# Optimization experiments

Hardware: AMD Instinct MI355X
Metric: run time of the kernel (lower is better)

## Reference

```python
import jax, jax.numpy as jnp
import numpy as np

B, J, C = 4096, 17, 512       # batch, joints (length), channels (dim)
K, TOK, CH, H, KS, G = 3, 64, 1024, 8, 3, 8  # adj kernels, tokens_dim, channels_dim, heads, conv_large, gn groups
EPS = 1e-5


def setup_inputs() -> dict:
    key = jax.random.key(0)
    ks = jax.random.split(key, 16)
    r = lambda i, shp, s=0.02: jax.random.normal(ks[i], shp, jnp.float32) * s
    return {
        "x": jax.random.normal(ks[0], (B, J, C), jnp.float32),
        "adj": jax.random.uniform(ks[1], (K, J, J), jnp.float32) / J,
        "norm1_w": jnp.ones((J,), jnp.float32), "norm1_b": jnp.zeros((J,), jnp.float32),
        "gcn1_w": r(2, (K * C, C)), "gcn1_b": jnp.zeros((K * C,), jnp.float32),
        "dw_w": r(3, (C, 1, KS), 0.1), "dw_b": jnp.zeros((C,), jnp.float32),
        "gn1_w": jnp.ones((C,), jnp.float32), "gn1_b": jnp.zeros((C,), jnp.float32),
        "pw_w": r(4, (C, C)), "pw_b": jnp.zeros((C,), jnp.float32),
        "mlp1_w1": r(5, (TOK, J)), "mlp1_b1": jnp.zeros((TOK,), jnp.float32),
        "mlp1_w2": r(6, (J, TOK)), "mlp1_b2": jnp.zeros((J,), jnp.float32),
        "qkv_w": r(7, (3 * C, C)), "qkv_b": jnp.zeros((3 * C,), jnp.float32),
        "proj_w": r(8, (C, C)), "proj_b": jnp.zeros((C,), jnp.float32),
        "gnf_w": jnp.ones((C,), jnp.float32), "gnf_b": jnp.zeros((C,), jnp.float32),
        "norm2_w": jnp.ones((C,), jnp.float32), "norm2_b": jnp.zeros((C,), jnp.float32),
        "mlp2_w1": r(9, (CH, C)), "mlp2_b1": jnp.zeros((CH,), jnp.float32),
        "mlp2_w2": r(10, (C, CH)), "mlp2_b2": jnp.zeros((C,), jnp.float32),
        "gcn2_w": r(11, (K * C, C)), "gcn2_b": jnp.zeros((K * C,), jnp.float32),
    }


def _gelu(t):
    return jax.nn.gelu(t, approximate=False)  # torch nn.GELU default is exact erf


def _ln(t, w, b):  # LayerNorm over last axis
    m = t.mean(-1, keepdims=True)
    v = ((t - m) ** 2).mean(-1, keepdims=True)
    return (t - m) * jax.lax.rsqrt(v + EPS) * w + b


def _gn(t, w, b):  # GroupNorm(G, C) over (B, C, J)
    Bn, Cc, Jn = t.shape
    r = t.reshape(Bn, G, -1)
    m = r.mean(-1, keepdims=True)
    v = ((r - m) ** 2).mean(-1, keepdims=True)
    r = (r - m) * jax.lax.rsqrt(v + EPS)
    return r.reshape(Bn, Cc, Jn) * w[:, None] + b[:, None]


def _gcn(t, w, b, adj):  # t: (B,C,J); 1x1 conv to K*C then einsum with adj (K,J,J)
    y = jnp.einsum('bcj,oc->boj', t, w) + b[:, None]
    y = y.reshape(t.shape[0], K, C, t.shape[2])
    return jnp.einsum('bkcv,kvw->bcw', y, adj)


def reference(x, adj, norm1_w, norm1_b, gcn1_w, gcn1_b, dw_w, dw_b, gn1_w, gn1_b,
              pw_w, pw_b, mlp1_w1, mlp1_b1, mlp1_w2, mlp1_b2, qkv_w, qkv_b,
              proj_w, proj_b, gnf_w, gnf_b, norm2_w, norm2_b,
              mlp2_w1, mlp2_b1, mlp2_w2, mlp2_b2, gcn2_w, gcn2_b):
    res = x                                   # (B,J,C)
    xc = jnp.swapaxes(x, 1, 2)                # (B,C,J)
    xc = _ln(xc, norm1_w, norm1_b)            # LayerNorm over joints

    # --- branch 1: GCN ---
    x_gcn1 = _gcn(xc, gcn1_w, gcn1_b, adj)    # (B,C,J)

    # --- branch 2: depthwise conv + token MLP ---
    h = jax.lax.conv_general_dilated(xc, dw_w, (1,), [(KS // 2, KS // 2)],
                                     dimension_numbers=('NCH', 'OIH', 'NCH'),
                                     feature_group_count=C) + dw_b[:, None]
    h = _gelu(_gn(h, gn1_w, gn1_b))
    h = jnp.einsum('bcj,oc->boj', h, pw_w) + pw_b[:, None]      # 1x1 conv
    h = _gelu(jnp.einsum('bcj,tj->bct', h, mlp1_w1) + mlp1_b1)  # token mlp fc1
    h = jnp.einsum('bct,jt->bcj', h, mlp1_w2) + mlp1_b2         # token mlp fc2

    # --- branch 3: global spatial attention over joints ---
    dh = C // H
    qkv = jnp.einsum('bcj,oc->boj', xc, qkv_w) + qkv_b[:, None]  # (B,3C,J)
    q, k_, v_ = jnp.split(qkv, 3, axis=1)
    q = q.reshape(-1, H, dh, J); k_ = k_.reshape(-1, H, dh, J); v_ = v_.reshape(-1, H, dh, J)
    attn = jax.nn.softmax(jnp.einsum('bhdi,bhdj->bhij', q, k_) / jnp.sqrt(jnp.float32(dh)), axis=-1)
    sga = jnp.einsum('bhij,bhdj->bhdi', attn, v_).reshape(-1, C, J)
    sga = jnp.einsum('bcj,oc->boj', sga, proj_w) + proj_b[:, None]

    # --- fuse ---
    xc = _gelu(_gn(sga + x_gcn1 + h, gnf_w, gnf_b))
    xj = jnp.swapaxes(xc, 1, 2)               # (B,J,C)
    res_channel = xj
    xn = _ln(xj + res, norm2_w, norm2_b)      # LayerNorm over channels
    m = _gelu(jnp.einsum('bjc,hc->bjh', xn, mlp2_w1) + mlp2_b1)
    m = jnp.einsum('bjh,ch->bjc', m, mlp2_w2) + mlp2_b2
    g2 = _gcn(jnp.swapaxes(m, 1, 2), gcn2_w, gcn2_b, adj)  # (B,C,J)
    xj = res_channel + jnp.swapaxes(g2, 1, 2)
    return xj + res
```

## Files before the change

### kernel.cpp

```cpp
#include <hip/hip_runtime.h>
#include <stdint.h>

#define BB 4096
#define JJ 17
#define CC 512

typedef unsigned short u16;
typedef __bf16 bf16x8 __attribute__((ext_vector_type(8)));
typedef float  f32x4  __attribute__((ext_vector_type(4)));
typedef float  f32x2  __attribute__((ext_vector_type(2)));

__device__ __forceinline__ float bf2f(u16 u){ return __uint_as_float(((uint32_t)u)<<16); }
__device__ __forceinline__ u16 f2bf(float f){
  uint32_t u = __float_as_uint(f);
  u += 0x7fffu + ((u>>16)&1u);
  return (u16)(u>>16);
}
__device__ __forceinline__ void unpk2(uint32_t u, float& lo, float& hi){
  lo = __uint_as_float(u<<16);
  hi = __uint_as_float(u & 0xffff0000u);
}
__device__ __forceinline__ float gelu_f(float x){
  float x2 = x*x;
  float y2 = x*fmaf(0.0713548162726f, x2, 1.59576912161f);
  float ey = __builtin_amdgcn_exp2f(y2*1.44269504089f);
  return fmaf(-x, __builtin_amdgcn_rcpf(ey+1.f), x);
}
__device__ __forceinline__ void pkfma(f32x2& d, f32x2 a, f32x2 b){
  asm volatile("v_pk_fma_f32 %0, %1, %2, %0" : "+v"(d) : "v"(a), "v"(b));
}
__device__ __forceinline__ void gll16(const void* g, void* l){
  __builtin_amdgcn_global_load_lds(
      (const __attribute__((address_space(1))) void*)g,
      (__attribute__((address_space(3))) void*)l, 16, 0, 0);
}

__global__ void k_cvt(const float* __restrict__ in, u16* __restrict__ out, int n){
  int i = blockIdx.x*blockDim.x + threadIdx.x;
  if (i < n) out[i] = f2bf(in[i]);
}

__global__ void k_tokprep(const float* __restrict__ w1, const float* __restrict__ w2,
                          float* __restrict__ w1p, float* __restrict__ w2p){
  int i = blockIdx.x*blockDim.x + threadIdx.x;
  if (i >= 1280) return;
  int t = i/20, j = i%20;
  w1p[i] = (j<17) ? w1[t*17+j] : 0.f;
  w2p[i] = (j<17) ? w2[j*64+t] : 0.f;
}

__global__ __launch_bounds__(512) void k_pre(
    const float* __restrict__ x, int b0,
    const float* __restrict__ n1w, const float* __restrict__ n1b,
    const float* __restrict__ dww, const float* __restrict__ dwb,
    const float* __restrict__ gn1w, const float* __restrict__ gn1b,
    u16* __restrict__ xc, u16* __restrict__ hgn)
{
  int b = blockIdx.x, c = threadIdx.x;
  const float* xp = x + (size_t)(b0+b)*JJ*CC + c;
  float v[JJ]; float s = 0.f;
  #pragma unroll
  for (int j=0;j<JJ;j++){ v[j] = xp[(size_t)j*CC]; s += v[j]; }
  float mn = s*(1.f/JJ); float var = 0.f;
  #pragma unroll
  for (int j=0;j<JJ;j++){ float d=v[j]-mn; var += d*d; }
  float rr = rsqrtf(var*(1.f/JJ)+1e-5f);
  float xcv[JJ];
  #pragma unroll
  for (int j=0;j<JJ;j++) xcv[j] = (v[j]-mn)*rr*n1w[j] + n1b[j];
  u16* xo = xc + (size_t)b*JJ*CC + c;
  #pragma unroll
  for (int j=0;j<JJ;j++) xo[(size_t)j*CC] = f2bf(xcv[j]);
  float w0=dww[c*3+0], w1=dww[c*3+1], w2=dww[c*3+2], db=dwb[c];
  float h[JJ];
  #pragma unroll
  for (int j=0;j<JJ;j++){
    float a = db + w1*xcv[j];
    if (j>0)    a += w0*xcv[j-1];
    if (j<JJ-1) a += w2*xcv[j+1];
    h[j] = a;
  }
  float ss=0.f, sq=0.f;
  #pragma unroll
  for (int j=0;j<JJ;j++){ ss += h[j]; sq += h[j]*h[j]; }
  for (int off=32; off; off>>=1){ ss += __shfl_xor(ss,off); sq += __shfl_xor(sq,off); }
  float gm = ss*(1.f/(64.f*JJ));
  float gr = rsqrtf(sq*(1.f/(64.f*JJ)) - gm*gm + 1e-5f);
  float gw = gn1w[c], gb = gn1b[c];
  u16* ho = hgn + (size_t)b*JJ*CC + c;
  #pragma unroll
  for (int j=0;j<JJ;j++){
    float t = (h[j]-gm)*gr*gw + gb;
    ho[(size_t)j*CC] = f2bf(gelu_f(t));
  }
}

template<int DO_GELU, int DO_ADD>
__global__ __launch_bounds__(512,2) void gemm256(
    const u16* __restrict__ A, const u16* __restrict__ W, const float* __restrict__ bias,
    u16* __restrict__ out, const u16* __restrict__ add0, const u16* __restrict__ add1,
    int M, int N, int K, int NXT)
{
  __shared__ __align__(16) u16 lds[65536];
  const int tid  = threadIdx.x;
  const int wid  = tid>>6, lane = tid&63;

  const int nwg = gridDim.x;
  const int q8 = nwg>>3, r8 = nwg&7;
  const int xcd = blockIdx.x & 7, sub = blockIdx.x >> 3;
  const int wg = (xcd<r8 ? xcd*(q8+1) : r8*(q8+1)+(xcd-r8)*q8) + sub;
  const int n0 = (wg % NXT)*256;
  const int m0 = (wg / NXT)*256;

  const int wm = wid>>2, wn = wid&3;
  const int lr = lane&15, lg = lane>>4;
  const int T  = K>>6;
  const int K64 = K<<6;

  const int rg = tid>>3, g = tid&7;
  const int gswS = (g ^ (rg&7))<<3;
  const u16* gA = A + (size_t)(m0+rg)*K + gswS;
  const u16* gB = W + (size_t)(n0+rg)*K + gswS;
  const int stl = wid*512;

  const int gsw0 = ((0+lg) ^ (lr&7))<<3;
  const int gsw1 = ((4+lg) ^ (lr&7))<<3;
  const int rowA0 = wm*128 + lr;
  const int rowB0 = wn*64  + lr;

  f32x4 acc[8][4];
  #pragma unroll
  for (int i=0;i<8;i++)
    #pragma unroll
    for (int j=0;j<4;j++) acc[i][j] = (f32x4){0.f,0.f,0.f,0.f};

  bf16x8 av[2][4], bv0[2][2], bv1[2][2];

  auto STAGE = [&](const u16* ga, const u16* gb, int bufo){
    u16* la = lds + bufo + stl;
    u16* lb = lds + 32768 + bufo + stl;
    gll16(ga,        la);
    gll16(ga+K64,    la+4096);
    gll16(ga+2*K64,  la+8192);
    gll16(ga+3*K64,  la+12288);
    gll16(gb,        lb);
    gll16(gb+K64,    lb+4096);
    gll16(gb+2*K64,  lb+8192);
    gll16(gb+3*K64,  lb+12288);
  };
  auto LDA = [&](int qm, int bufo){
    #pragma unroll
    for (int i=0;i<4;i++){
      const int rb = bufo + (rowA0 + qm*64 + i*16)*64;
      av[0][i] = *(const bf16x8*)&lds[rb + gsw0];
      av[1][i] = *(const bf16x8*)&lds[rb + gsw1];
    }
  };
  auto LDB = [&](int qn, int bufo, bf16x8 (&bv)[2][2]){
    #pragma unroll
    for (int j=0;j<2;j++){
      const int rb = 32768 + bufo + (rowB0 + qn*32 + j*16)*64;
      bv[0][j] = *(const bf16x8*)&lds[rb + gsw0];
      bv[1][j] = *(const bf16x8*)&lds[rb + gsw1];
    }
  };
  auto MF = [&](int qm, int qn, bf16x8 (&bv)[2][2]){
    __builtin_amdgcn_s_setprio(1);
    #pragma unroll
    for (int kk=0;kk<2;kk++)
      #pragma unroll
      for (int i=0;i<4;i++)
        #pragma unroll
        for (int j=0;j<2;j++)
          acc[qm*4+i][qn*2+j] = __builtin_amdgcn_mfma_f32_16x16x32_bf16(
              av[kk][i], bv[kk][j], acc[qm*4+i][qn*2+j], 0,0,0);
    __builtin_amdgcn_s_setprio(0);
  };

  STAGE(gA, gB, 0);
  asm volatile("s_waitcnt vmcnt(0)" ::: "memory");
  __builtin_amdgcn_s_barrier();
  __builtin_amdgcn_sched_barrier(0);

  const u16* gAn = gA + 64;
  const u16* gBn = gB + 64;
  for (int t=0; t<T; ++t){
    const int bufo = (t&1)<<14;
    if (t+1 < T){
      STAGE(gAn, gBn, ((t+1)&1)<<14);
      gAn += 64; gBn += 64;
    }
    LDA(0, bufo); LDB(0, bufo, bv0);
    asm volatile("s_waitcnt lgkmcnt(0)" ::: "memory");
    __builtin_amdgcn_sched_barrier(0);
    MF(0,0,bv0);
    __builtin_amdgcn_s_barrier();
    LDB(1, bufo, bv1);
    asm volatile("s_waitcnt lgkmcnt(0)" ::: "memory");
    __builtin_amdgcn_sched_barrier(0);
    MF(0,1,bv1);
    __builtin_amdgcn_s_barrier();
    LDA(1, bufo);
    asm volatile("s_waitcnt lgkmcnt(0)" ::: "memory");
    __builtin_amdgcn_sched_barrier(0);
    MF(1,0,bv0);
    __builtin_amdgcn_s_barrier();
    MF(1,1,bv1);
    asm volatile("s_waitcnt vmcnt(0)" ::: "memory");
    __builtin_amdgcn_s_barrier();
    __builtin_amdgcn_sched_barrier(0);
  }

  const int rbase = lg*4;
  #pragma unroll
  for (int mi=0; mi<8; mi++){
    #pragma unroll
    for (int ni=0; ni<4; ni++){
      const int col  = n0 + wn*64 + ni*16 + lr;
      const int row0 = m0 + wm*128 + mi*16 + rbase;
      const float bvl = bias[col];
      #pragma unroll
      for (int r=0;r<4;r++){
        size_t idx = (size_t)(row0+r)*N + col;
        float v = acc[mi][ni][r] + bvl;
        if (DO_ADD)  v += bf2f(add0[idx]) + bf2f(add1[idx]);
        if (DO_GELU) v = gelu_f(v);
        out[idx] = f2bf(v);
      }
    }
  }
}

template<int FINAL>
__global__ __launch_bounds__(512) void k_gcn2(
    const u16* __restrict__ G, const float* __restrict__ adj,
    u16* __restrict__ xg,
    const u16* __restrict__ rc, const float* __restrict__ x, int b0,
    float* __restrict__ out)
{
  __shared__ __align__(16) float adjp[51*20];
  const int tid = threadIdx.x;
  for (int i=tid; i<1020; i+=512){
    int r=i/20, cl=i%20;
    adjp[i] = (cl<17) ? adj[r*17+cl] : 0.f;
  }
  __syncthreads();

  const int sl  = tid>>7;
  const int l   = tid&127;
  const int c0  = l*4;
  const int bl  = blockIdx.x*4 + sl;

  float acc[JJ][4];
  #pragma unroll
  for (int w=0;w<JJ;w++)
    #pragma unroll
    for (int e=0;e<4;e++) acc[w][e]=0.f;

  const u16* gbase = G + (size_t)bl*JJ*1536 + c0;
  #pragma unroll 3
  for (int kv=0; kv<51; kv++){
    const int k = kv/JJ, v = kv - k*JJ;
    uint2 yu = *(const uint2*)(gbase + (size_t)v*1536 + k*512);
    float y0,y1,y2,y3;
    unpk2(yu.x, y0, y1);
    unpk2(yu.y, y2, y3);
    const f32x4* arow = (const f32x4*)&adjp[kv*20];
    f32x4 a0=arow[0], a1=arow[1], a2=arow[2], a3=arow[3];
    float a16 = adjp[kv*20+16];
    float ar[JJ] = {a0[0],a0[1],a0[2],a0[3], a1[0],a1[1],a1[2],a1[3],
                    a2[0],a2[1],a2[2],a2[3], a3[0],a3[1],a3[2],a3[3], a16};
    #pragma unroll
    for (int w=0;w<JJ;w++){
      acc[w][0] += y0*ar[w];
      acc[w][1] += y1*ar[w];
      acc[w][2] += y2*ar[w];
      acc[w][3] += y3*ar[w];
    }
  }

  if (FINAL==0){
    u16* xo = xg + (size_t)bl*JJ*CC + c0;
    #pragma unroll
    for (int w=0;w<JJ;w++){
      uint2 o;
      o.x = (uint32_t)f2bf(acc[w][0]) | ((uint32_t)f2bf(acc[w][1])<<16);
      o.y = (uint32_t)f2bf(acc[w][2]) | ((uint32_t)f2bf(acc[w][3])<<16);
      *(uint2*)(xo + (size_t)w*CC) = o;
    }
  } else {
    const size_t gb = (size_t)(b0+bl)*JJ*CC + c0;
    const u16* rp = rc + (size_t)bl*JJ*CC + c0;
    #pragma unroll
    for (int w=0;w<JJ;w++){
      uint2 ru = *(const uint2*)(rp + (size_t)w*CC);
      float r0,r1,r2,r3;
      unpk2(ru.x, r0, r1);
      unpk2(ru.y, r2, r3);
      f32x4 xv = *(const f32x4*)(x + gb + (size_t)w*CC);
      f32x4 o;
      o[0]=acc[w][0]+r0+xv[0]; o[1]=acc[w][1]+r1+xv[1];
      o[2]=acc[w][2]+r2+xv[2]; o[3]=acc[w][3]+r3+xv[3];
      *(f32x4*)(out + gb + (size_t)w*CC) = o;
    }
  }
}

__global__ __launch_bounds__(512) void k_attn(const u16* __restrict__ Gqkv, u16* __restrict__ sga){
  __shared__ __align__(16) u16 qs[8*17*72];
  __shared__ __align__(16) u16 ks_[8*17*72];
  __shared__ __align__(16) float at[8*17*20];
  int b = blockIdx.x, tid = threadIdx.x;
  int h = tid>>6, d = tid&63;
  const u16* base = Gqkv + (size_t)b*JJ*1536;
  float vv[JJ];
  #pragma unroll
  for (int i=0;i<JJ;i++){
    qs [(h*JJ+i)*72 + d] = base[(size_t)i*1536 +        h*64 + d];
    ks_[(h*JJ+i)*72 + d] = base[(size_t)i*1536 +  512 + h*64 + d];
    vv[i] = bf2f(base[(size_t)i*1536 + 1024 + h*64 + d]);
  }
  __syncthreads();
  for (int p=d; p<289; p+=64){
    int i=p/JJ, j=p-i*JJ;
    const u16* qrow = &qs [(h*JJ+i)*72];
    const u16* krow = &ks_[(h*JJ+j)*72];
    float a=0.f;
    #pragma unroll
    for (int t=0;t<8;t++){
      bf16x8 q8 = *(const bf16x8*)&qrow[t*8];
      bf16x8 k8 = *(const bf16x8*)&krow[t*8];
      #pragma unroll
      for (int e=0;e<8;e++) a += (float)q8[e]*(float)k8[e];
    }
    at[(h*JJ+i)*20 + j] = a*0.125f;
  }
  __syncthreads();
  if (d < JJ){
    float* row = &at[(h*JJ+d)*20];
    f32x4 r0=((f32x4*)row)[0], r1=((f32x4*)row)[1], r2=((f32x4*)row)[2], r3=((f32x4*)row)[3];
    float e16=row[16];
    float rv[JJ]={r0[0],r0[1],r0[2],r0[3],r1[0],r1[1],r1[2],r1[3],
                  r2[0],r2[1],r2[2],r2[3],r3[0],r3[1],r3[2],r3[3],e16};
    float mx=-1e30f;
    #pragma unroll
    for (int j=0;j<JJ;j++) mx=fmaxf(mx,rv[j]);
    float sm=0.f;
    #pragma unroll
    for (int j=0;j<JJ;j++){ rv[j]=__builtin_amdgcn_exp2f((rv[j]-mx)*1.44269504089f); sm+=rv[j]; }
    float inv=1.f/sm;
    #pragma unroll
    for (int j=0;j<JJ;j++) row[j]=rv[j]*inv;
  }
  __syncthreads();
  #pragma unroll
  for (int i=0;i<JJ;i++){
    const float* row = &at[(h*JJ+i)*20];
    f32x4 r0=((const f32x4*)row)[0], r1=((const f32x4*)row)[1],
          r2=((const f32x4*)row)[2], r3=((const f32x4*)row)[3];
    float a = r0[0]*vv[0]+r0[1]*vv[1]+r0[2]*vv[2]+r0[3]*vv[3]
            + r1[0]*vv[4]+r1[1]*vv[5]+r1[2]*vv[6]+r1[3]*vv[7]
            + r2[0]*vv[8]+r2[1]*vv[9]+r2[2]*vv[10]+r2[3]*vv[11]
            + r3[0]*vv[12]+r3[1]*vv[13]+r3[2]*vv[14]+r3[3]*vv[15]
            + row[16]*vv[16];
    sga[((size_t)b*JJ+i)*CC + h*64 + d] = f2bf(a);
  }
}

__global__ __launch_bounds__(512) void k_tok(const u16* __restrict__ Hpw,
    const float* __restrict__ w1p, const float* __restrict__ w2p,
    const float* __restrict__ b1, const float* __restrict__ b2,
    u16* __restrict__ h2o){
  __shared__ __align__(16) float w1s[1280], w2s[1280];
  __shared__ float b1s[64], b2s[20];
  const int tid = threadIdx.x;
  for (int i=tid; i<1280; i+=512){ w1s[i]=w1p[i]; w2s[i]=w2p[i]; }
  if (tid<64) b1s[tid]=b1[tid];
  if (tid<20) b2s[tid] = (tid<17) ? b2[tid] : 0.f;
  __syncthreads();

  const int bl = blockIdx.x*2 + (tid>>8);
  const int c0 = tid&255;
  const u16* hp = Hpw + (size_t)bl*JJ*CC;
  float hv0[JJ], hv1[JJ];
  #pragma unroll
  for (int j=0;j<JJ;j++){
    hv0[j]=bf2f(hp[(size_t)j*CC + c0]);
    hv1[j]=bf2f(hp[(size_t)j*CC + c0 + 256]);
  }
  f32x2 h0p[9], h1p[9];
  #pragma unroll
  for (int p=0;p<8;p++){
    h0p[p] = (f32x2){hv0[2*p], hv0[2*p+1]};
    h1p[p] = (f32x2){hv1[2*p], hv1[2*p+1]};
  }
  h0p[8] = (f32x2){hv0[16], 0.f};
  h1p[8] = (f32x2){hv1[16], 0.f};

  f32x2 a20[9], a21[9];
  #pragma unroll
  for (int p=0;p<9;p++){
    f32x2 bb = (f32x2){b2s[2*p], b2s[2*p+1]};
    a20[p]=bb; a21[p]=bb;
  }

  for (int t=0;t<64;t++){
    f32x4 wa = *(const f32x4*)&w1s[t*20];
    f32x4 wb = *(const f32x4*)&w1s[t*20+4];
    f32x4 wc = *(const f32x4*)&w1s[t*20+8];
    f32x4 wd = *(const f32x4*)&w1s[t*20+12];
    float  we = w1s[t*20+16];
    f32x2 wp[9] = {(f32x2){wa[0],wa[1]},(f32x2){wa[2],wa[3]},
                   (f32x2){wb[0],wb[1]},(f32x2){wb[2],wb[3]},
                   (f32x2){wc[0],wc[1]},(f32x2){wc[2],wc[3]},
                   (f32x2){wd[0],wd[1]},(f32x2){wd[2],wd[3]},
                   (f32x2){we,0.f}};
    f32x2 s0 = (f32x2){b1s[t], 0.f};
    f32x2 s1 = s0;
    #pragma unroll
    for (int p=0;p<9;p++){ pkfma(s0, h0p[p], wp[p]); pkfma(s1, h1p[p], wp[p]); }
    float a0 = gelu_f(s0[0] + s0[1]);
    float a1 = gelu_f(s1[0] + s1[1]);
    wa = *(const f32x4*)&w2s[t*20];
    wb = *(const f32x4*)&w2s[t*20+4];
    wc = *(const f32x4*)&w2s[t*20+8];
    wd = *(const f32x4*)&w2s[t*20+12];
    we = w2s[t*20+16];
    f32x2 wq[9] = {(f32x2){wa[0],wa[1]},(f32x2){wa[2],wa[3]},
                   (f32x2){wb[0],wb[1]},(f32x2){wb[2],wb[3]},
                   (f32x2){wc[0],wc[1]},(f32x2){wc[2],wc[3]},
                   (f32x2){wd[0],wd[1]},(f32x2){wd[2],wd[3]},
                   (f32x2){we,0.f}};
    f32x2 a0b = (f32x2){a0,a0};
    f32x2 a1b = (f32x2){a1,a1};
    #pragma unroll
    for (int p=0;p<9;p++){ pkfma(a20[p], a0b, wq[p]); pkfma(a21[p], a1b, wq[p]); }
  }
  u16* ho = h2o + (size_t)bl*JJ*CC;
  #pragma unroll
  for (int j=0;j<JJ;j++){
    ho[(size_t)j*CC + c0]       = f2bf(a20[j>>1][j&1]);
    ho[(size_t)j*CC + c0 + 256] = f2bf(a21[j>>1][j&1]);
  }
}

__global__ __launch_bounds__(512) void k_fuse(const u16* __restrict__ s,
    const float* __restrict__ x, int b0,
    const float* __restrict__ gfw, const float* __restrict__ gfb,
    const float* __restrict__ n2w, const float* __restrict__ n2b,
    u16* __restrict__ rc, u16* __restrict__ xn){
  __shared__ float rS[8][JJ], rQ[8][JJ];
  int b = blockIdx.x, c = threadIdx.x;
  int wave = c>>6, lane = c&63;
  const u16* sp = s + (size_t)b*JJ*CC + c;
  float sv[JJ];
  #pragma unroll
  for (int j=0;j<JJ;j++) sv[j]=bf2f(sp[(size_t)j*CC]);
  float ss=0.f, sq=0.f;
  #pragma unroll
  for (int j=0;j<JJ;j++){ ss+=sv[j]; sq+=sv[j]*sv[j]; }
  for (int off=32; off; off>>=1){ ss += __shfl_xor(ss,off); sq += __shfl_xor(sq,off); }
  float gm = ss*(1.f/1088.f);
  float gr = rsqrtf(sq*(1.f/1088.f) - gm*gm + 1e-5f);
  float gw=gfw[c], gb=gfb[c];
  const float* xp = x + (size_t)(b0+b)*JJ*CC + c;
  u16* rp = rc + (size_t)b*JJ*CC + c;
  float t[JJ];
  #pragma unroll
  for (int j=0;j<JJ;j++){
    float v = gelu_f((sv[j]-gm)*gr*gw + gb);
    rp[(size_t)j*CC] = f2bf(v);
    t[j] = v + xp[(size_t)j*CC];
  }
  #pragma unroll
  for (int j=0;j<JJ;j++){
    float a=t[j], q=a*a;
    for (int off=32; off; off>>=1){ a+=__shfl_xor(a,off); q+=__shfl_xor(q,off); }
    if (lane==0){ rS[wave][j]=a; rQ[wave][j]=q; }
  }
  __syncthreads();
  float wN=n2w[c], bN=n2b[c];
  u16* xo = xn + (size_t)b*JJ*CC + c;
  #pragma unroll
  for (int j=0;j<JJ;j++){
    float S=0.f,Q=0.f;
    #pragma unroll
    for (int w=0;w<8;w++){ S+=rS[w][j]; Q+=rQ[w][j]; }
    float mn=S*(1.f/512.f);
    float r2=rsqrtf(Q*(1.f/512.f)-mn*mn+1e-5f);
    xo[(size_t)j*CC]=f2bf((t[j]-mn)*r2*wN+bN);
  }
}

extern "C" void kernel_launch(void* const* d_in, const int* in_sizes, int n_in,
                              void* d_out, int out_size, void* d_ws, size_t ws_size,
                              hipStream_t stream)
{
  const float* x      = (const float*)d_in[0];
  const float* adj    = (const float*)d_in[1];
  const float* n1w    = (const float*)d_in[2];
  const float* n1b    = (const float*)d_in[3];
  const float* gcn1_w = (const float*)d_in[4];
  const float* gcn1_b = (const float*)d_in[5];
  const float* dw_w   = (const float*)d_in[6];
  const float* dw_b   = (const float*)d_in[7];
  const float* gn1_w  = (const float*)d_in[8];
  const float* gn1_b  = (const float*)d_in[9];
  const float* pw_w   = (const float*)d_in[10];
  const float* pw_b   = (const float*)d_in[11];
  const float* m1w1   = (const float*)d_in[12];
  const float* m1b1   = (const float*)d_in[13];
  const float* m1w2   = (const float*)d_in[14];
  const float* m1b2   = (const float*)d_in[15];
  const float* qkv_w  = (const float*)d_in[16];
  const float* qkv_b  = (const float*)d_in[17];
  const float* proj_w = (const float*)d_in[18];
  const float* proj_b = (const float*)d_in[19];
  const float* gnf_w  = (const float*)d_in[20];
  const float* gnf_b  = (const float*)d_in[21];
  const float* n2w    = (const float*)d_in[22];
  const float* n2b    = (const float*)d_in[23];
  const float* m2w1   = (const float*)d_in[24];
  const float* m2b1   = (const float*)d_in[25];
  const float* m2w2   = (const float*)d_in[26];
  const float* m2b2   = (const float*)d_in[27];
  const float* gcn2_w = (const float*)d_in[28];
  const float* gcn2_b = (const float*)d_in[29];
  float* out = (float*)d_out;

  char* ws = (char*)d_ws;
  const size_t WBYTES = (size_t)3932160*2;
  const size_t TPBYTES = 2560*4;

  const int cands[5] = {4096,2048,1024,512,256};
  int NB = 0;
  for (int ci=0; ci<5; ci++){
    size_t need = WBYTES + TPBYTES + (size_t)cands[ci]*JJ*2*(1536 + 4*512);
    if (need <= ws_size){ NB = cands[ci]; break; }
  }
  if (NB == 0) return;

  u16* wb = (u16*)ws;
  float* w1p = (float*)(ws + WBYTES);
  float* w2p = w1p + 1280;
  char* p = ws + WBYTES + TPBYTES;
  const size_t SZ_BIGc = (size_t)NB*JJ*1536*2;
  const size_t SZTc    = (size_t)NB*JJ*512*2;
  u16* big = (u16*)p;               p += SZ_BIGc;
  u16* t0  = (u16*)p;               p += SZTc;
  u16* t1  = (u16*)p;               p += SZTc;
  u16* t2  = (u16*)p;               p += SZTc;
  u16* t3  = (u16*)p;

  u16 *wg1=wb, *wqkv=wb+786432, *wpw=wb+1572864, *wproj=wb+1835008,
      *wm1=wb+2097152, *wm2=wb+2621440, *wg2=wb+3145728;

  k_cvt<<<(786432+255)/256,256,0,stream>>>(gcn1_w,wg1,786432);
  k_cvt<<<(786432+255)/256,256,0,stream>>>(qkv_w,wqkv,786432);
  k_cvt<<<(262144+255)/256,256,0,stream>>>(pw_w,wpw,262144);
  k_cvt<<<(262144+255)/256,256,0,stream>>>(proj_w,wproj,262144);
  k_cvt<<<(524288+255)/256,256,0,stream>>>(m2w1,wm1,524288);
  k_cvt<<<(524288+255)/256,256,0,stream>>>(m2w2,wm2,524288);
  k_cvt<<<(786432+255)/256,256,0,stream>>>(gcn2_w,wg2,786432);
  k_tokprep<<<5,256,0,stream>>>(m1w1,m1w2,w1p,w2p);

  const int M2 = NB*JJ;
  const int MT = M2/256;
  for (int b0 = 0; b0 < BB; b0 += NB){
    k_pre<<<NB,512,0,stream>>>(x,b0,n1w,n1b,dw_w,dw_b,gn1_w,gn1_b, t0, t1);
    gemm256<0,0><<<MT*6,512,0,stream>>>(t0,wg1,gcn1_b,big,nullptr,nullptr,M2,1536,512,6);
    k_gcn2<0><<<NB/4,512,0,stream>>>(big,adj,t2,nullptr,nullptr,0,nullptr);
    gemm256<0,0><<<MT*6,512,0,stream>>>(t0,wqkv,qkv_b,big,nullptr,nullptr,M2,1536,512,6);
    k_attn<<<NB,512,0,stream>>>(big,t3);
    gemm256<0,0><<<MT*2,512,0,stream>>>(t1,wpw,pw_b,t0,nullptr,nullptr,M2,512,512,2);
    k_tok<<<NB/2,512,0,stream>>>(t0,w1p,w2p,m1b1,m1b2,t1);
    gemm256<0,1><<<MT*2,512,0,stream>>>(t3,wproj,proj_b,t0,t2,t1,M2,512,512,2);
    k_fuse<<<NB,512,0,stream>>>(t0,x,b0,gnf_w,gnf_b,n2w,n2b,t1,t2);
    gemm256<1,0><<<MT*4,512,0,stream>>>(t2,wm1,m2b1,big,nullptr,nullptr,M2,1024,512,4);
    gemm256<0,0><<<MT*2,512,0,stream>>>(big,wm2,m2b2,t0,nullptr,nullptr,M2,512,1024,2);
    gemm256<0,0><<<MT*6,512,0,stream>>>(t0,wg2,gcn2_b,big,nullptr,nullptr,M2,1536,512,6);
    k_gcn2<1><<<NB/4,512,0,stream>>>(big,adj,nullptr,t1,x,b0,out);
  }
}
```

Before: 1.449 ms.

## Replace 256x256 double-buffered GEMM with 128x128 triple-buffered K=32 pipeline

Rewrites the bf16 MFMA GEMM to use 128x128 tiles with 256 threads, BK=32 and a three-stage LDS ring buffer that prefetches two steps ahead. Each wave computes a 64x64 block with a single load/compute phase per K step instead of four barrier-separated sub-phases. Smaller tiles and 48KB of LDS allow three workgroups per CU and a larger grid, trading lower per-tile data reuse and more global traffic for better occupancy and latency hiding.

```diff
diff --git a/kernel.cpp b/kernel.cpp
--- a/kernel.cpp
+++ b/kernel.cpp
@@ -96,133 +96,94 @@
 }
 
 template<int DO_GELU, int DO_ADD>
-__global__ __launch_bounds__(512,2) void gemm256(
+__global__ __launch_bounds__(256,3) void gemm_r3(
     const u16* __restrict__ A, const u16* __restrict__ W, const float* __restrict__ bias,
     u16* __restrict__ out, const u16* __restrict__ add0, const u16* __restrict__ add1,
     int M, int N, int K, int NXT)
 {
-  __shared__ __align__(16) u16 lds[65536];
-  const int tid  = threadIdx.x;
-  const int wid  = tid>>6, lane = tid&63;
+  __shared__ __align__(16) u16 lds[24576];
+  const int tid = threadIdx.x;
+  const int wid = tid>>6, lane = tid&63;
 
   const int nwg = gridDim.x;
   const int q8 = nwg>>3, r8 = nwg&7;
   const int xcd = blockIdx.x & 7, sub = blockIdx.x >> 3;
   const int wg = (xcd<r8 ? xcd*(q8+1) : r8*(q8+1)+(xcd-r8)*q8) + sub;
-  const int n0 = (wg % NXT)*256;
-  const int m0 = (wg / NXT)*256;
-
-  const int wm = wid>>2, wn = wid&3;
+  const int n0 = (wg % NXT)*128;
+  const int m0 = (wg / NXT)*128;
+
+  const int wm = wid>>1, wn = wid&1;
   const int lr = lane&15, lg = lane>>4;
-  const int T  = K>>6;
+  const int T  = K>>5;
+
+  const int srow = tid>>2;
+  const int gswS = ((tid&3) ^ ((tid>>3)&3))<<3;
+  const u16* gA = A + (size_t)(m0+srow)*K + gswS;
+  const u16* gB = W + (size_t)(n0+srow)*K + gswS;
   const int K64 = K<<6;
-
-  const int rg = tid>>3, g = tid&7;
-  const int gswS = (g ^ (rg&7))<<3;
-  const u16* gA = A + (size_t)(m0+rg)*K + gswS;
-  const u16* gB = W + (size_t)(n0+rg)*K + gswS;
-  const int stl = wid*512;
-
-  const int gsw0 = ((0+lg) ^ (lr&7))<<3;
-  const int gsw1 = ((4+lg) ^ (lr&7))<<3;
-  const int rowA0 = wm*128 + lr;
-  const int rowB0 = wn*64  + lr;
-
-  f32x4 acc[8][4];
-  #pragma unroll
-  for (int i=0;i<8;i++)
+  const int dstl = tid*8;
+
+  const int g8 = (lg ^ ((lr>>1)&3))<<3;
+  const int offA0 = (wm*64+lr)*32 + g8;
+  const int offB0 = 4096 + (wn*64+lr)*32 + g8;
+
+  f32x4 acc[4][4];
+  #pragma unroll
+  for (int i=0;i<4;i++)
     #pragma unroll
     for (int j=0;j<4;j++) acc[i][j] = (f32x4){0.f,0.f,0.f,0.f};
 
-  bf16x8 av[2][4], bv0[2][2], bv1[2][2];
-
-  auto STAGE = [&](const u16* ga, const u16* gb, int bufo){
-    u16* la = lds + bufo + stl;
-    u16* lb = lds + 32768 + bufo + stl;
-    gll16(ga,        la);
-    gll16(ga+K64,    la+4096);
-    gll16(ga+2*K64,  la+8192);
-    gll16(ga+3*K64,  la+12288);
-    gll16(gb,        lb);
-    gll16(gb+K64,    lb+4096);
-    gll16(gb+2*K64,  lb+8192);
-    gll16(gb+3*K64,  lb+12288);
+  auto STAGE = [&](int t, int sofs){
+    const u16* ga = gA + t*32;
+    const u16* gb = gB + t*32;
+    u16* la = lds + sofs + dstl;
+    u16* lb = lds + sofs + 4096 + dstl;
+    gll16(ga,     la);
+    gll16(ga+K64, la+2048);
+    gll16(gb,     lb);
+    gll16(gb+K64, lb+2048);
   };
-  auto LDA = [&](int qm, int bufo){
-    #pragma unroll
-    for (int i=0;i<4;i++){
-      const int rb = bufo + (rowA0 + qm*64 + i*16)*64;
-      av[0][i] = *(const bf16x8*)&lds[rb + gsw0];
-      av[1][i] = *(const bf16x8*)&lds[rb + gsw1];
-    }
-  };
-  auto LDB = [&](int qn, int bufo, bf16x8 (&bv)[2][2]){
-    #pragma unroll
-    for (int j=0;j<2;j++){
-      const int rb = 32768 + bufo + (rowB0 + qn*32 + j*16)*64;
-      bv[0][j] = *(const bf16x8*)&lds[rb + gsw0];
-      bv[1][j] = *(const bf16x8*)&lds[rb + gsw1];
-    }
-  };
-  auto MF = [&](int qm, int qn, bf16x8 (&bv)[2][2]){
-    __builtin_amdgcn_s_setprio(1);
-    #pragma unroll
-    for (int kk=0;kk<2;kk++)
-      #pragma unroll
-      for (int i=0;i<4;i++)
-        #pragma unroll
-        for (int j=0;j<2;j++)
-          acc[qm*4+i][qn*2+j] = __builtin_amdgcn_mfma_f32_16x16x32_bf16(
-              av[kk][i], bv[kk][j], acc[qm*4+i][qn*2+j], 0,0,0);
-    __builtin_amdgcn_s_setprio(0);
-  };
-
-  STAGE(gA, gB, 0);
-  asm volatile("s_waitcnt vmcnt(0)" ::: "memory");
+
+  STAGE(0, 0); STAGE(1, 8192);
+  asm volatile("s_waitcnt vmcnt(4)" ::: "memory");
   __builtin_amdgcn_s_barrier();
-  __builtin_amdgcn_sched_barrier(0);
-
-  const u16* gAn = gA + 64;
-  const u16* gBn = gB + 64;
+
+  int s0 = 0, s1 = 8192, s2 = 16384;
   for (int t=0; t<T; ++t){
-    const int bufo = (t&1)<<14;
-    if (t+1 < T){
-      STAGE(gAn, gBn, ((t+1)&1)<<14);
-      gAn += 64; gBn += 64;
-    }
-    LDA(0, bufo); LDB(0, bufo, bv0);
+    const bool more = (t+2 < T);
+    if (more) STAGE(t+2, s2);
+    bf16x8 av[4], bv[4];
+    #pragma unroll
+    for (int i=0;i<4;i++) av[i] = *(const bf16x8*)&lds[s0 + offA0 + i*512];
+    #pragma unroll
+    for (int j=0;j<4;j++) bv[j] = *(const bf16x8*)&lds[s0 + offB0 + j*512];
     asm volatile("s_waitcnt lgkmcnt(0)" ::: "memory");
     __builtin_amdgcn_sched_barrier(0);
-    MF(0,0,bv0);
+    __builtin_amdgcn_s_setprio(1);
+    #pragma unroll
+    for (int i=0;i<4;i++)
+      #pragma unroll
+      for (int j=0;j<4;j++)
+        acc[i][j] = __builtin_amdgcn_mfma_f32_16x16x32_bf16(av[i], bv[j], acc[i][j], 0,0,0);
+    __builtin_amdgcn_s_setprio(0);
+    if (more) asm volatile("s_waitcnt vmcnt(4)" ::: "memory");
+    else      asm volatile("s_waitcnt vmcnt(0)" ::: "memory");
     __builtin_amdgcn_s_barrier();
-    LDB(1, bufo, bv1);
-    asm volatile("s_waitcnt lgkmcnt(0)" ::: "memory");
-    __builtin_amdgcn_sched_barrier(0);
-    MF(0,1,bv1);
-    __builtin_amdgcn_s_barrier();
-    LDA(1, bufo);
-    asm volatile("s_waitcnt lgkmcnt(0)" ::: "memory");
-    __builtin_amdgcn_sched_barrier(0);
-    MF(1,0,bv0);
-    __builtin_amdgcn_s_barrier();
-    MF(1,1,bv1);
-    asm volatile("s_waitcnt vmcnt(0)" ::: "memory");
-    __builtin_amdgcn_s_barrier();
-    __builtin_amdgcn_sched_barrier(0);
+    const int tmp = s0; s0 = s1; s1 = s2; s2 = tmp;
   }
 
   const int rbase = lg*4;
   #pragma unroll
-  for (int mi=0; mi<8; mi++){
-    #pragma unroll
-    for (int ni=0; ni<4; ni++){
-      const int col  = n0 + wn*64 + ni*16 + lr;
-      const int row0 = m0 + wm*128 + mi*16 + rbase;
+  for (int i=0;i<4;i++){
+    #pragma unroll
+    for (int j=0;j<4;j++){
+      const int col  = n0 + wn*64 + j*16 + lr;
+      const int row0 = m0 + wm*64 + i*16 + rbase;
       const float bvl = bias[col];
       #pragma unroll
       for (int r=0;r<4;r++){
         size_t idx = (size_t)(row0+r)*N + col;
-        float v = acc[mi][ni][r] + bvl;
+        float v = acc[i][j][r] + bvl;
         if (DO_ADD)  v += bf2f(add0[idx]) + bf2f(add1[idx]);
         if (DO_GELU) v = gelu_f(v);
         out[idx] = f2bf(v);
@@ -565,20 +526,20 @@
   k_tokprep<<<5,256,0,stream>>>(m1w1,m1w2,w1p,w2p);
 
   const int M2 = NB*JJ;
-  const int MT = M2/256;
+  const int MT = M2/128;
   for (int b0 = 0; b0 < BB; b0 += NB){
     k_pre<<<NB,512,0,stream>>>(x,b0,n1w,n1b,dw_w,dw_b,gn1_w,gn1_b, t0, t1);
-    gemm256<0,0><<<MT*6,512,0,stream>>>(t0,wg1,gcn1_b,big,nullptr,nullptr,M2,1536,512,6);
+    gemm_r3<0,0><<<MT*12,256,0,stream>>>(t0,wg1,gcn1_b,big,nullptr,nullptr,M2,1536,512,12);
     k_gcn2<0><<<NB/4,512,0,stream>>>(big,adj,t2,nullptr,nullptr,0,nullptr);
-    gemm256<0,0><<<MT*6,512,0,stream>>>(t0,wqkv,qkv_b,big,nullptr,nullptr,M2,1536,512,6);
+    gemm_r3<0,0><<<MT*12,256,0,stream>>>(t0,wqkv,qkv_b,big,nullptr,nullptr,M2,1536,512,12);
     k_attn<<<NB,512,0,stream>>>(big,t3);
-    gemm256<0,0><<<MT*2,512,0,stream>>>(t1,wpw,pw_b,t0,nullptr,nullptr,M2,512,512,2);
+    gemm_r3<0,0><<<MT*4,256,0,stream>>>(t1,wpw,pw_b,t0,nullptr,nullptr,M2,512,512,4);
     k_tok<<<NB/2,512,0,stream>>>(t0,w1p,w2p,m1b1,m1b2,t1);
-    gemm256<0,1><<<MT*2,512,0,stream>>>(t3,wproj,proj_b,t0,t2,t1,M2,512,512,2);
+    gemm_r3<0,1><<<MT*4,256,0,stream>>>(t3,wproj,proj_b,t0,t2,t1,M2,512,512,4);
     k_fuse<<<NB,512,0,stream>>>(t0,x,b0,gnf_w,gnf_b,n2w,n2b,t1,t2);
-    gemm256<1,0><<<MT*4,512,0,stream>>>(t2,wm1,m2b1,big,nullptr,nullptr,M2,1024,512,4);
-    gemm256<0,0><<<MT*2,512,0,stream>>>(big,wm2,m2b2,t0,nullptr,nullptr,M2,512,1024,2);
-    gemm256<0,0><<<MT*6,512,0,stream>>>(t0,wg2,gcn2_b,big,nullptr,nullptr,M2,1536,512,6);
+    gemm_r3<1,0><<<MT*8,256,0,stream>>>(t2,wm1,m2b1,big,nullptr,nullptr,M2,1024,512,8);
+    gemm_r3<0,0><<<MT*4,256,0,stream>>>(big,wm2,m2b2,t0,nullptr,nullptr,M2,512,1024,4);
+    gemm_r3<0,0><<<MT*12,256,0,stream>>>(t0,wg2,gcn2_b,big,nullptr,nullptr,M2,1536,512,12);
     k_gcn2<1><<<NB/4,512,0,stream>>>(big,adj,nullptr,t1,x,b0,out);
   }
 }
```

Result: faster. 1.420 ms (-2.0%).
